# Kernel tuning notes

Hardware: AMD Instinct MI355X
Metric: run time of the kernel (lower is better)

## Reference

```python
import jax, jax.numpy as jnp
import numpy as np
import math

B, C, H, W = 16, 256, 32, 32
MPHI = 16      # GRModule projection channels
NNODE = 20     # symbol nodes
DEMB = 300     # fastText dim


def setup_inputs() -> dict:
    key = jax.random.key(0)
    ks = jax.random.split(key, 24)
    r = lambda i, shp, s=0.05: jax.random.normal(ks[i], shp, dtype=jnp.float32) * s
    return {
        'x': r(0, (B, C, H, W), 1.0),
        'emb': r(1, (NNODE, DEMB), 1.0),
        'adj': jax.random.uniform(ks[2], (NNODE, NNODE), dtype=jnp.float32),
        'wq': r(3, (DEMB, DEMB)), 'bq': r(4, (DEMB,)),
        'wk': r(5, (DEMB, DEMB)), 'bk': r(6, (DEMB,)),
        'wv': r(7, (DEMB, DEMB)), 'bv': r(8, (DEMB,)),
        'wo': r(9, (DEMB, DEMB)), 'bo': r(10, (DEMB,)),
        'phi_w': r(11, (MPHI, C)), 'phi_b': r(12, (MPHI,)),
        'glob_w': r(13, (MPHI, C)),
        'gc1_w': r(14, (DEMB, C)),
        'gc2_w': r(15, (C, C)),
        'gw_w': r(16, (C, C)),
        's2l_w': r(17, (2 * C,)), 's2l_b': r(18, (1,)),
        'final_w': r(19, (C, 2 * C)),
    }


def _attention_graph(node, wq, bq, wk, bk, wv, bv, wo, bo):
    # node: [N, 300]. Single-head self-attention, mean-pooled residual (dropout=eval).
    q = node @ wq + bq
    k = node @ wk + bk
    v = node @ wv + bv
    att = jax.nn.softmax(q @ k.T / math.sqrt(DEMB), axis=-1)
    node1 = (att @ v).mean(axis=0, keepdims=True)      # [1, 300]
    node2 = node1 @ wo + bo
    return node + node2                                 # broadcast residual


def _gr_module(x, phi_w, phi_b, glob_w):
    # x: [B, C, H, W] -> [B, HW, C]
    b = x.shape[0]
    phi = jnp.einsum('oc,bchw->bohw', phi_w, x) + phi_b[None, :, None, None]  # [B,16,H,W]
    x_phi = jax.nn.relu(phi.reshape(b, -1, MPHI))       # raw reshape, as in torch .view
    x_phi_T = jax.nn.relu(phi.reshape(b, MPHI, -1))
    g = jnp.einsum('oc,bc->bo', glob_w, x.mean(axis=(2, 3)))  # [B,16]
    # sigmoid of the diag-embedded matrix: off-diagonal becomes sigmoid(0)=0.5 (faithful)
    Dg = jax.nn.sigmoid(jax.vmap(jnp.diag)(g))          # [B,16,16]
    A = jax.nn.softmax(jnp.einsum('bpm,bmn,bnq->bpq', x_phi, Dg, x_phi_T), axis=-1)
    d = 1.0 / jnp.sqrt(A.sum(axis=2))
    d = jnp.where(jnp.isfinite(d), d, 0.0)              # nan/inf -> 0
    L = jnp.eye(A.shape[1], dtype=A.dtype) - d[:, :, None] * A * d[:, None, :]
    return jnp.einsum('bpq,bqc->bpc', L, x.reshape(b, -1, x.shape[1]))


def _normalize_adjacency(adj):
    a_hat = adj + jnp.eye(adj.shape[0], dtype=adj.dtype)
    d = 1.0 / jnp.sqrt(a_hat.sum(axis=1))
    d = jnp.where(jnp.isfinite(d), d, 0.0)
    return d[:, None] * a_hat * d[None, :]


def reference(x, emb, adj, wq, bq, wk, bk, wv, bv, wo, bo,
              phi_w, phi_b, glob_w, gc1_w, gc2_w, gw_w, s2l_w, s2l_b, final_w):
    b, c, h, w = x.shape
    # --- semantic branch: attention over word graph + 2-layer GCN ---
    ev = _attention_graph(emb, wq, bq, wk, bk, wv, bv, wo, bo)  # [N,300]
    ev = jnp.broadcast_to(ev[None], (b, NNODE, DEMB))
    adj_n = _normalize_adjacency(adj)                   # [N,N]
    g1 = jax.nn.relu(jnp.einsum('pq,bqd->bpd', adj_n, ev @ gc1_w))   # [B,N,256]
    g2 = jax.nn.relu(jnp.einsum('pq,bqd->bpd', adj_n, g1 @ gc2_w))   # [B,N,256]
    # --- local branch: GRModule Laplacian smoothing + 1x1 conv ---
    spiral = _gr_module(x, phi_w, phi_b, glob_w)        # [B,HW,C]
    spiral_map = spiral.reshape(b, h, w, c).transpose(0, 3, 1, 2)    # [B,C,H,W]
    local = jnp.einsum('oc,bchw->bohw', gw_w, spiral_map)
    # --- semantic-to-local mapping (1x1 conv over concat == two dot products) ---
    inp_flat = x.transpose(0, 2, 3, 1).reshape(b, h * w, c)          # [B,HW,C]
    w_in, w_ev = s2l_w[:c], s2l_w[c:]
    logits = (inp_flat @ w_in)[:, :, None] + (g2 @ w_ev)[:, None, :] + s2l_b[0]
    mapping = jax.nn.softmax(logits, axis=1)            # softmax over pixels
    app = jax.nn.relu(jnp.einsum('bpm,bmc->bpc', mapping, g2))       # [B,HW,C]
    app = app.reshape(b, h, w, c).transpose(0, 3, 1, 2)              # [B,C,H,W]
    # --- fuse ---
    fused = jnp.concatenate([local, app], axis=1)       # [B,2C,H,W]
    out = jnp.einsum('oc,bchw->bohw', final_w, fused)
    return jax.nn.relu(out + x)
```

## Files before the change

kernel.cpp:

```cpp
#include <hip/hip_runtime.h>
#include <hip/hip_bf16.h>

typedef __bf16 bf16_t;
typedef bf16_t bf16x8 __attribute__((ext_vector_type(8)));
typedef bf16_t bf16x4 __attribute__((ext_vector_type(4)));
typedef float  f32x4  __attribute__((ext_vector_type(4)));

#define MFMA(a,b,c) __builtin_amdgcn_mfma_f32_16x16x32_bf16((a),(b),(c),0,0,0)

__global__ __launch_bounds__(256) void k_front(
    const float* final_w, const float* gw_w, const float* emb,
    const float* wq, const float* bq, const float* wk, const float* bk,
    const float* wv, const float* bvv, const float* x,
    const float* phi_w, const float* phi_b, const float* s2l_w,
    const float* gc1_w, const float* wo, const float* bo,
    bf16_t* M16, float* qkv, bf16_t* fB, bf16_t* fBT, float* s_raw,
    float* xsump, float* csum, float* fmaxp, float* cmaxp, bf16_t* xT,
    float* E1, float* WG1, float* bg1) {
  __shared__ __align__(16) char sp[27648];
  int bid = blockIdx.x, t = threadIdx.x;
  if (bid < 256) {
    float* fw = (float*)sp;
    int o = bid, c = t;
    fw[c] = final_w[o*512 + c];
    __syncthreads();
    float acc = 0.f;
    for (int k = 0; k < 256; ++k) acc += fw[k] * gw_w[k*256 + c];
    M16[o*256 + c] = (bf16_t)acc;
    return;
  }
  if (bid < 316) {
    int id = bid - 256;
    int mat = id / 20, row = id % 20;
    const float* W  = mat == 0 ? wq : (mat == 1 ? wk : wv);
    const float* Bb = mat == 0 ? bq : (mat == 1 ? bk : bvv);
    float* er = (float*)sp;
    for (int i = t; i < 300; i += 256) er[i] = emb[row*300 + i];
    __syncthreads();
    for (int o = t; o < 300; o += 256) {
      float acc = Bb[o];
      for (int d = 0; d < 300; ++d) acc += er[d] * W[d*300 + o];
      qkv[(mat*20 + row)*300 + o] = acc;
    }
    return;
  }
  if (bid < 444) {
    int id = bid - 316;
    int b = id >> 3, role = id & 7;
    const float* xb = x + b*262144;
    float* pw = (float*)sp;
    float* wi = pw + 4096;
    float* pb = wi + 256;
    float* phs = pb + 16;
    unsigned* fmu = (unsigned*)(phs + 2304);
    unsigned* cmu = fmu + 16;
    for (int i = t; i < 4096; i += 256) pw[i] = phi_w[i];
    wi[t] = s2l_w[t];
    if (t < 16) { pb[t] = phi_b[t]; fmu[t] = 0u; }
    if (t == 0) cmu[0] = 0u;
    __syncthreads();
    int hwl = t & 127, half = t >> 7;
    int hw = role*128 + hwl;
    float ph[16];
    #pragma unroll
    for (int o = 0; o < 16; ++o) ph[o] = 0.f;
    float sacc = 0.f;
    for (int ci = 0; ci < 128; ++ci) {
      int c = half*128 + ci;
      float xv = xb[c*1024 + hw];
      sacc += wi[c] * xv;
      #pragma unroll
      for (int o = 0; o < 16; ++o) ph[o] += pw[o*256 + c] * xv;
    }
    if (half == 0) {
      #pragma unroll
      for (int o = 0; o < 16; ++o) phs[hwl*18 + o] = ph[o];
      phs[hwl*18 + 16] = sacc;
    }
    __syncthreads();
    if (half == 1) {
      #pragma unroll
      for (int o = 0; o < 16; ++o) phs[hwl*18 + o] += ph[o];
      s_raw[b*1024 + hw] = phs[hwl*18 + 16] + sacc;
    }
    __syncthreads();
    float csacc = 0.f;
    #pragma unroll
    for (int i = 0; i < 8; ++i) {
      int j = i*256 + t;
      int o = j >> 7, hl = j & 127;
      float val = fmaxf(phs[hl*18 + o] + pb[o], 0.f);
      bf16_t bv16 = (bf16_t)val;
      atomicMax(&fmu[o], __float_as_uint((float)bv16));
      fB [b*16384 + o*1024 + role*128 + hl] = bv16;
      fBT[b*16384 + (role*128 + hl)*16 + o] = bv16;
      csacc += (float)bv16;
    }
    if (half == 0) phs[hwl*18 + 17] = csacc;
    __syncthreads();
    if (half == 1) {
      float cs = phs[hwl*18 + 17] + csacc;
      csum[b*1024 + hw] = cs;
      atomicMax(cmu, __float_as_uint(cs));
    }
    if (t < 16) fmaxp[b*128 + role*16 + t] = __uint_as_float(fmu[t]);
    __syncthreads();
    if (t == 0) cmaxp[b*8 + role] = __uint_as_float(cmu[0]);
    {
      const f32x4* xr = (const f32x4*)(xb + t*1024 + role*128);
      float s4 = 0.f;
      #pragma unroll
      for (int j = 0; j < 32; ++j) { f32x4 v = xr[j]; s4 += v[0] + v[1] + v[2] + v[3]; }
      xsump[(b*8 + role)*256 + t] = s4;
    }
    return;
  }
  if (bid < 464) {
    int n = bid - 444;
    float* er = (float*)sp;
    for (int i = t; i < 300; i += 256) er[i] = emb[n*300 + i];
    __syncthreads();
    float acc = 0.f;
    for (int d = 0; d < 300; ++d) acc += er[d] * gc1_w[d*256 + t];
    E1[n*256 + t] = acc;
    return;
  }
  if (bid < 765) {
    int d0 = bid - 464;
    float* er = (float*)sp;
    if (d0 < 300) { for (int i = t; i < 300; i += 256) er[i] = wo[d0*300 + i]; }
    else          { for (int i = t; i < 300; i += 256) er[i] = bo[i]; }
    __syncthreads();
    float acc = 0.f;
    for (int e = 0; e < 300; ++e) acc += er[e] * gc1_w[e*256 + t];
    if (d0 < 300) WG1[d0*256 + t] = acc; else bg1[t] = acc;
    return;
  }
  {
    int id = bid - 765;
    int bb = id >> 6, tile = id & 63;
    int q0 = (tile >> 2) * 64, c0 = (tile & 3) * 64;
    bf16_t* tl = (bf16_t*)sp;
    const float* xbb = x + bb*262144;
    #pragma unroll
    for (int k = 0; k < 16; ++k) {
      int idx = k*256 + t, qi = idx >> 6, ci = idx & 63;
      tl[ci*74 + qi] = (bf16_t)xbb[(q0 + qi)*256 + c0 + ci];
    }
    __syncthreads();
    #pragma unroll
    for (int k = 0; k < 16; ++k) {
      int idx = k*256 + t, ci = idx >> 6, qi = idx & 63;
      xT[bb*262144 + (c0 + ci)*1024 + q0 + qi] = tl[ci*74 + qi];
    }
    return;
  }
}

__global__ __launch_bounds__(512) void k_mid1(
    const float* adj, const float* qkv, const float* E1,
    const float* glob_w, const float* xsump, const float* s_raw,
    const float* fmaxp, const float* cmaxp,
    float* n1g, float* adjng, float* rsAg, float* AE1g,
    float* dgd, float* mcol, float* fmaxb, float* cmaxb) {
  __shared__ __align__(16) float sp[12480];
  int t = threadIdx.x;
  if (blockIdx.x == 0) {
    float* A  = sp;
    float* Bs = A + 6000;
    float* att  = Bs + 6000;
    float* wsum = att + 400;
    for (int i = t; i < 6000; i += 512) { A[i] = qkv[i]; Bs[i] = qkv[6000 + i]; }
    __syncthreads();
    if (t < 400) {
      int i = t / 20, j = t % 20;
      float acc = 0.f;
      for (int d = 0; d < 300; ++d) acc += A[i*300 + d] * Bs[j*300 + d];
      att[t] = acc * 0.05773502691896258f;
    }
    __syncthreads();
    if (t < 20) {
      float m = -1e30f;
      for (int j = 0; j < 20; ++j) m = fmaxf(m, att[t*20 + j]);
      float s = 0.f;
      for (int j = 0; j < 20; ++j) { float e = __expf(att[t*20 + j] - m); att[t*20 + j] = e; s += e; }
      float inv = 1.f / s;
      for (int j = 0; j < 20; ++j) att[t*20 + j] *= inv;
    }
    __syncthreads();
    if (t < 20) {
      float s = 0.f;
      for (int i = 0; i < 20; ++i) s += att[i*20 + t];
      wsum[t] = s * 0.05f;
    }
    __syncthreads();
    if (t < 300) {
      const float* v = qkv + 12000;
      float acc = 0.f;
      for (int j = 0; j < 20; ++j) acc += wsum[j] * v[j*300 + t];
      n1g[t] = acc;
    }
    return;
  }
  if (blockIdx.x == 1) {
    float* drt = sp;
    float* an  = sp + 32;
    if (t < 20) {
      float s = 1.f;
      for (int j = 0; j < 20; ++j) s += adj[t*20 + j];
      drt[t] = rsqrtf(s);
    }
    __syncthreads();
    if (t < 400) {
      int i = t / 20, j = t % 20;
      float a = adj[t] + (i == j ? 1.f : 0.f);
      float v = drt[i] * a * drt[j];
      an[t] = v;
      adjng[t] = v;
    }
    __syncthreads();
    if (t < 20) {
      float s = 0.f;
      for (int m = 0; m < 20; ++m) s += an[t*20 + m];
      rsAg[t] = s;
    }
    if (t < 256) {
      float e[20];
      #pragma unroll
      for (int m = 0; m < 20; ++m) e[m] = E1[m*256 + t];
      for (int n = 0; n < 20; ++n) {
        float acc = 0.f;
        #pragma unroll
        for (int m = 0; m < 20; ++m) acc += an[n*20 + m] * e[m];
        AE1g[n*256 + t] = acc;
      }
    }
    return;
  }
  int b = blockIdx.x - 2;
  float* xm = sp;
  float* redm = xm + 256;
  float* reds = redm + 8;
  if (t < 256) {
    float s = 0.f;
    #pragma unroll
    for (int r = 0; r < 8; ++r) s += xsump[(b*8 + r)*256 + t];
    xm[t] = s * (1.f / 1024.f);
  }
  if (t >= 256 && t < 272) {
    int m = t - 256; float fm = 0.f;
    for (int r = 0; r < 8; ++r) fm = fmaxf(fm, fmaxp[b*128 + r*16 + m]);
    fmaxb[b*16 + m] = fm;
  }
  if (t == 272) {
    float cm = 0.f;
    for (int r = 0; r < 8; ++r) cm = fmaxf(cm, cmaxp[b*8 + r]);
    cmaxb[b] = cm;
  }
  __syncthreads();
  if (t < 16) {
    float g = 0.f;
    for (int c = 0; c < 256; ++c) g += glob_w[t*256 + c] * xm[c];
    dgd[b*16 + t] = 0.5f * tanhf(0.5f * g);
  }
  float v0 = s_raw[b*1024 + t], v1 = s_raw[b*1024 + 512 + t];
  float m = fmaxf(v0, v1);
  #pragma unroll
  for (int off = 32; off; off >>= 1) m = fmaxf(m, __shfl_xor(m, off, 64));
  int wv = t >> 6, ll = t & 63;
  if (ll == 0) redm[wv] = m;
  __syncthreads();
  float bm = redm[0];
  #pragma unroll
  for (int i = 1; i < 8; ++i) bm = fmaxf(bm, redm[i]);
  float e0 = __expf(v0 - bm), e1 = __expf(v1 - bm);
  float s2 = e0 + e1;
  #pragma unroll
  for (int off = 32; off; off >>= 1) s2 += __shfl_xor(s2, off, 64);
  if (ll == 0) reds[wv] = s2;
  __syncthreads();
  float tot = 0.f;
  #pragma unroll
  for (int i = 0; i < 8; ++i) tot += reds[i];
  float inv = 1.f / tot;
  mcol[b*1024 + t]       = e0 * inv;
  mcol[b*1024 + 512 + t] = e1 * inv;
}

__global__ __launch_bounds__(256) void k_w1(const float* n1g, const float* WG1,
                                            float* w1part) {
  int t = threadIdx.x, i = blockIdx.x, d0 = i*8;
  float acc = 0.f;
  #pragma unroll
  for (int k = 0; k < 8; ++k) {
    int d = d0 + k;
    if (d < 300) acc += n1g[d] * WG1[d*256 + t];
  }
  w1part[i*256 + t] = acc;
}

__global__ __launch_bounds__(256) void k_gu(const float* w1part,
    const float* bg1, const float* AE1g, const float* rsAg, const float* adjng,
    const float* gc2_w, const float* final_w, float* upart) {
  __shared__ float adjns[400], rsAs[32], w1s[256], h2s[640], rgs[32];
  __shared__ float g1s[5120];
  int t = threadIdx.x, c0 = blockIdx.x * 32;
  for (int i = t; i < 400; i += 256) adjns[i] = adjng[i];
  if (t < 20) rsAs[t] = rsAg[t];
  {
    float acc = bg1[t];
    #pragma unroll
    for (int i = 0; i < 38; ++i) acc += w1part[i*256 + t];
    w1s[t] = acc;
  }
  __syncthreads();
  for (int i = t; i < 5120; i += 256) {
    int n = i >> 8;
    g1s[i] = fmaxf(AE1g[i] + rsAs[n] * w1s[i & 255], 0.f);
  }
  __syncthreads();
  int cl = t & 31, ng = t >> 5;
  float a0 = 0.f, a1 = 0.f, a2 = 0.f;
  for (int d = 0; d < 256; ++d) {
    float wv = gc2_w[d*256 + c0 + cl];
    a0 += g1s[ng*256 + d] * wv;
    a1 += g1s[(ng + 8)*256 + d] * wv;
    if (ng < 4) a2 += g1s[(ng + 16)*256 + d] * wv;
  }
  h2s[ng*32 + cl] = a0;
  h2s[(ng + 8)*32 + cl] = a1;
  if (ng < 4) h2s[(ng + 16)*32 + cl] = a2;
  __syncthreads();
  if (t < 32) {
    float rga = 0.f;
    for (int n = 0; n < 20; ++n) {
      float acc = 0.f;
      #pragma unroll
      for (int m = 0; m < 20; ++m) acc += adjns[n*20 + m] * h2s[m*32 + t];
      rga += fmaxf(acc, 0.f);
    }
    rgs[t] = rga;
  }
  __syncthreads();
  {
    float acc = 0.f;
    const float* fw = final_w + t*512 + 256 + c0;
    #pragma unroll
    for (int kk = 0; kk < 32; ++kk) acc += fw[kk] * rgs[kk];
    upart[blockIdx.x*256 + t] = acc;
  }
}

__global__ __launch_bounds__(256) void k_main(const float* x, const bf16_t* fB,
    const bf16_t* fBT, const bf16_t* xT, const bf16_t* M16, const float* fmaxb,
    const float* mcol, const float* upart, const float* dgd, const float* csum,
    const float* cmaxb, float* out) {
  int flat = blockIdx.y * 32 + blockIdx.x;
  int b  = (flat & 7) * 2 + ((flat >> 3) >> 5);
  int p0 = ((flat >> 3) & 31) * 32;
  int t = threadIdx.x, w = t >> 6, l = t & 63, lr = l & 15, quad = l >> 4;
  int qh = w >> 1, ph = w & 1;
  __shared__ __align__(16) char smem[16896];
  bf16_t* PT0  = (bf16_t*)smem;
  bf16_t* e_s  = (bf16_t*)(smem + 10240);
  bf16_t* T_ls = (bf16_t*)smem;
  __shared__ float Mb_s[32], fmax_s[16], u_s[256], rsinv_s[32], dgd_s[16];
  __shared__ float c_s[1024], ha_s[32], rs_s[2][32];
  const float*  xb   = x   + b*262144;
  const bf16_t* fBb  = fB  + b*16384;
  const bf16_t* fBTb = fBT + b*16384;
  const bf16_t* xTb  = xT  + b*262144;
  for (int i = t; i < 1280; i += 256) e_s[i] = (bf16_t)0.f;
  {
    float us = 0.f;
    #pragma unroll
    for (int j = 0; j < 8; ++j) us += upart[j*256 + t];
    u_s[t] = us;
  }
  for (int i = t; i < 1024; i += 256) c_s[i] = csum[b*1024 + i];
  if (t < 16) { fmax_s[t] = fmaxb[b*16 + t]; dgd_s[t] = dgd[b*16 + t]; }
  __syncthreads();
  for (int i = t; i < 512; i += 256) {
    int p = i >> 4, m = i & 15;
    e_s[p*40 + m] = (bf16_t)((float)fBb[p0*16 + i] * dgd_s[m]);
  }
  __syncthreads();
  if (t < 32) {
    float a = 0.f;
    #pragma unroll
    for (int m = 0; m < 16; ++m) a += (float)fBb[(p0 + t)*16 + m];
    float ha = 0.5f * a;
    ha_s[t] = ha;
    float mb = ha * cmaxb[b];
    #pragma unroll
    for (int m = 0; m < 16; ++m) mb += fmaxf((float)e_s[t*40 + m], 0.f) * fmax_s[m];
    Mb_s[t] = mb;
  }
  __syncthreads();
  bf16x8 be = *(const bf16x8*)(e_s + (ph*16 + lr)*40 + quad*8);
  float mb_lane = Mb_s[ph*16 + lr];
  float ha_lane = ha_s[ph*16 + lr];
  float rs = 0.f;
  f32x4 acc[2][4];
  #pragma unroll
  for (int i = 0; i < 2; ++i)
    #pragma unroll
    for (int j = 0; j < 4; ++j) acc[i][j] = (f32x4){0.f, 0.f, 0.f, 0.f};
  bf16x8 zer;
  #pragma unroll
  for (int j = 0; j < 8; ++j) zer[j] = (bf16_t)0.f;
  bf16x8 a0[2], a0n[2];
  a0[0] = a0[1] = a0n[0] = a0n[1] = zer;
  if (quad < 2) {
    a0[0] = *(const bf16x8*)(fBTb + (qh*16 + lr)*16 + quad*8);
    a0[1] = *(const bf16x8*)(fBTb + (32 + qh*16 + lr)*16 + quad*8);
  }
  const bf16_t* xrow = xTb + (w*64 + lr)*1024 + quad*8;
  bf16x8 bv[2][4], bvn[2][4];
  #pragma unroll
  for (int k = 0; k < 2; ++k)
    #pragma unroll
    for (int cf = 0; cf < 4; ++cf)
      bv[k][cf] = *(const bf16x8*)(xrow + cf*16384 + k*32);
  int cur = 0;
  for (int u2 = 0; u2 < 16; ++u2) {
    f32x4 z = {0.f, 0.f, 0.f, 0.f};
    f32x4 s0 = MFMA(a0[0], be, z);
    f32x4 s1 = MFMA(a0[1], be, z);
    if (u2 < 15) {
      if (quad < 2) {
        a0n[0] = *(const bf16x8*)(fBTb + ((u2*2 + 2)*32 + qh*16 + lr)*16 + quad*8);
        a0n[1] = *(const bf16x8*)(fBTb + ((u2*2 + 3)*32 + qh*16 + lr)*16 + quad*8);
      }
      #pragma unroll
      for (int k = 0; k < 2; ++k)
        #pragma unroll
        for (int cf = 0; cf < 4; ++cf)
          bvn[k][cf] = *(const bf16x8*)(xrow + cf*16384 + (u2*2 + 2 + k)*32);
    }
    bf16_t* PTc = PT0 + cur*2560;
    bf16x4 pv0, pv1;
    #pragma unroll
    for (int r = 0; r < 4; ++r) {
      float S0 = s0[r] + ha_lane * c_s[(u2*2)*32 + qh*16 + quad*4 + r];
      float E0 = __expf(S0 - mb_lane);
      rs += E0; pv0[r] = (bf16_t)E0;
      float S1 = s1[r] + ha_lane * c_s[(u2*2 + 1)*32 + qh*16 + quad*4 + r];
      float E1v = __expf(S1 - mb_lane);
      rs += E1v; pv1[r] = (bf16_t)E1v;
    }
    *(bf16x4*)(PTc + (ph*16 + lr)*40 + qh*16 + quad*4)        = pv0;
    *(bf16x4*)(PTc + 1280 + (ph*16 + lr)*40 + qh*16 + quad*4) = pv1;
    __syncthreads();
    #pragma unroll
    for (int k = 0; k < 2; ++k) {
      bf16x8 ap0 = *(const bf16x8*)(PTc + k*1280 + lr*40 + quad*8);
      bf16x8 ap1 = *(const bf16x8*)(PTc + k*1280 + (16 + lr)*40 + quad*8);
      #pragma unroll
      for (int cf = 0; cf < 4; ++cf) {
        acc[0][cf] = MFMA(ap0, bv[k][cf], acc[0][cf]);
        acc[1][cf] = MFMA(ap1, bv[k][cf], acc[1][cf]);
      }
    }
    if (u2 < 15) {
      #pragma unroll
      for (int k = 0; k < 2; ++k) {
        a0[k] = a0n[k];
        #pragma unroll
        for (int cf = 0; cf < 4; ++cf) bv[k][cf] = bvn[k][cf];
      }
    }
    cur ^= 1;
  }
  rs += __shfl_xor(rs, 16, 64);
  rs += __shfl_xor(rs, 32, 64);
  if (l < 16) rs_s[qh][ph*16 + lr] = rs;
  __syncthreads();
  if (t < 32) rsinv_s[t] = 1.f / fmaxf(rs_s[0][t] + rs_s[1][t], 1e-30f);
  __syncthreads();
  #pragma unroll
  for (int pf = 0; pf < 2; ++pf)
    #pragma unroll
    for (int cf = 0; cf < 4; ++cf)
      #pragma unroll
      for (int r = 0; r < 4; ++r) {
        int p = pf*16 + quad*4 + r;
        int c = w*64 + cf*16 + lr;
        float tv = xb[(p0 + p)*256 + c] - acc[pf][cf][r] * rsinv_s[p];
        T_ls[p*264 + c] = (bf16_t)tv;
      }
  __syncthreads();
  f32x4 acc2[4][2];
  #pragma unroll
  for (int i = 0; i < 4; ++i)
    #pragma unroll
    for (int j = 0; j < 2; ++j) acc2[i][j] = (f32x4){0.f, 0.f, 0.f, 0.f};
  for (int c0 = 0; c0 < 256; c0 += 32) {
    bf16x8 am[4], bt[2];
    #pragma unroll
    for (int of = 0; of < 4; ++of)
      am[of] = *(const bf16x8*)(M16 + (w*64 + of*16 + lr)*256 + c0 + quad*8);
    #pragma unroll
    for (int pf = 0; pf < 2; ++pf)
      bt[pf] = *(const bf16x8*)(T_ls + (pf*16 + lr)*264 + c0 + quad*8);
    #pragma unroll
    for (int of = 0; of < 4; ++of)
      #pragma unroll
      for (int pf = 0; pf < 2; ++pf) acc2[of][pf] = MFMA(am[of], bt[pf], acc2[of][pf]);
  }
  float* outb = out + b*262144;
  #pragma unroll
  for (int of = 0; of < 4; ++of)
    #pragma unroll
    for (int pf = 0; pf < 2; ++pf)
      #pragma unroll
      for (int r = 0; r < 4; ++r) {
        int o = w*64 + of*16 + quad*4 + r;
        int pg = p0 + pf*16 + lr;
        float v = acc2[of][pf][r] + mcol[b*1024 + pg] * u_s[o] + xb[o*1024 + pg];
        outb[o*1024 + pg] = fmaxf(v, 0.f);
      }
}


extern "C" void kernel_launch(void* const* d_in, const int* in_sizes, int n_in,
                              void* d_out, int out_size, void* d_ws, size_t ws_size,
                              hipStream_t stream) {
  (void)in_sizes; (void)n_in; (void)out_size; (void)ws_size;
  const float* x       = (const float*)d_in[0];
  const float* emb     = (const float*)d_in[1];
  const float* adj     = (const float*)d_in[2];
  const float* wq      = (const float*)d_in[3];
  const float* bq      = (const float*)d_in[4];
  const float* wk      = (const float*)d_in[5];
  const float* bk      = (const float*)d_in[6];
  const float* wv      = (const float*)d_in[7];
  const float* bv      = (const float*)d_in[8];
  const float* wo      = (const float*)d_in[9];
  const float* bo      = (const float*)d_in[10];
  const float* phi_w   = (const float*)d_in[11];
  const float* phi_b   = (const float*)d_in[12];
  const float* glob_w  = (const float*)d_in[13];
  const float* gc1_w   = (const float*)d_in[14];
  const float* gc2_w   = (const float*)d_in[15];
  const float* gw_w    = (const float*)d_in[16];
  const float* s2l_w   = (const float*)d_in[17];
  const float* final_w = (const float*)d_in[19];
  float* out = (float*)d_out;

  float* W = (float*)d_ws;
  float* qkv    = W + 0;
  float* xsump  = W + 18048;
  float* s_raw  = W + 50816;
  float* mcol   = W + 67200;
  float* fmaxb  = W + 83584;
  float* dgd    = W + 83840;
  float* csum   = W + 84096;
  float* cmaxb  = W + 100480;
  float* fmaxp  = W + 100544;
  float* cmaxp  = W + 102592;
  float* E1     = W + 102720;
  float* WG1    = W + 107840;
  float* bg1    = W + 184640;
  float* n1     = W + 184896;
  float* adjn   = W + 185216;
  float* rsA    = W + 185664;
  float* AE1    = W + 185728;
  float* upart  = W + 190848;
  float* w1part = W + 192896;
  bf16_t* M16 = (bf16_t*)((char*)d_ws + 851968);
  bf16_t* fB  = (bf16_t*)((char*)d_ws + 983040);
  bf16_t* fBT = (bf16_t*)((char*)d_ws + 1507328);
  bf16_t* xT  = (bf16_t*)((char*)d_ws + 2031616);

  k_front<<<1789, 256, 0, stream>>>(final_w, gw_w, emb, wq, bq, wk, bk, wv, bv, x,
                                    phi_w, phi_b, s2l_w, gc1_w, wo, bo,
                                    M16, qkv, fB, fBT, s_raw, xsump, csum,
                                    fmaxp, cmaxp, xT, E1, WG1, bg1);
  k_mid1<<<18, 512, 0, stream>>>(adj, qkv, E1, glob_w, xsump, s_raw,
                                 fmaxp, cmaxp,
                                 n1, adjn, rsA, AE1, dgd, mcol, fmaxb, cmaxb);
  k_w1<<<38, 256, 0, stream>>>(n1, WG1, w1part);
  k_gu<<<8, 256, 0, stream>>>(w1part, bg1, AE1, rsA, adjn, gc2_w, final_w, upart);
  k_main<<<dim3(32, 16), 256, 0, stream>>>(x, fB, fBT, xT, M16, fmaxb, mcol, upart,
                                           dgd, csum, cmaxb, out);
}
```

Measured before the change: 232.4 us.

## Split k_gu over more blocks; restructure k_main softmax-attention to per-wave register shuffles

k_gu now runs 32 blocks of 8 output columns each instead of 8 blocks of 32. It stages the gc2_w slice in shared memory and uses a padded g1 layout. k_main is reorganized so each wave owns a 16-pixel by 128-channel tile and computes all query steps itself. The exp'd attention probabilities are passed into the A operand through cross-lane shuffles instead of a shared-memory transpose with a block barrier each step, and row sums are reduced within the wave. In exchange it drops the software prefetch of the next step's operands and duplicates the score MFMA and exp work across the two channel-half waves.

```diff
diff --git a/kernel.cpp b/kernel.cpp
--- a/kernel.cpp
+++ b/kernel.cpp
@@ -302,42 +302,45 @@
 __global__ __launch_bounds__(256) void k_gu(const float* w1part,
     const float* bg1, const float* AE1g, const float* rsAg, const float* adjng,
     const float* gc2_w, const float* final_w, float* upart) {
-  __shared__ float adjns[400], rsAs[32], w1s[256], h2s[640], rgs[32];
-  __shared__ float g1s[5120];
-  int t = threadIdx.x, c0 = blockIdx.x * 32;
+  __shared__ float adjns[400], rsAs[32], w1s[256], h2s[176], rgs[8];
+  __shared__ float g1s[20*260];
+  __shared__ float gs2[2048];
+  int t = threadIdx.x, c0 = blockIdx.x * 8;
   for (int i = t; i < 400; i += 256) adjns[i] = adjng[i];
   if (t < 20) rsAs[t] = rsAg[t];
+  #pragma unroll
+  for (int k2 = 0; k2 < 8; ++k2) {
+    int idx = k2*256 + t, d = idx >> 3, cl = idx & 7;
+    gs2[idx] = gc2_w[d*256 + c0 + cl];
+  }
   {
     float acc = bg1[t];
     #pragma unroll
     for (int i = 0; i < 38; ++i) acc += w1part[i*256 + t];
     w1s[t] = acc;
   }
-  __syncthreads();
-  for (int i = t; i < 5120; i += 256) {
-    int n = i >> 8;
-    g1s[i] = fmaxf(AE1g[i] + rsAs[n] * w1s[i & 255], 0.f);
-  }
-  __syncthreads();
-  int cl = t & 31, ng = t >> 5;
-  float a0 = 0.f, a1 = 0.f, a2 = 0.f;
-  for (int d = 0; d < 256; ++d) {
-    float wv = gc2_w[d*256 + c0 + cl];
-    a0 += g1s[ng*256 + d] * wv;
-    a1 += g1s[(ng + 8)*256 + d] * wv;
-    if (ng < 4) a2 += g1s[(ng + 16)*256 + d] * wv;
-  }
-  h2s[ng*32 + cl] = a0;
-  h2s[(ng + 8)*32 + cl] = a1;
-  if (ng < 4) h2s[(ng + 16)*32 + cl] = a2;
-  __syncthreads();
-  if (t < 32) {
+  float ae[20];
+  #pragma unroll
+  for (int k2 = 0; k2 < 20; ++k2) ae[k2] = AE1g[k2*256 + t];
+  __syncthreads();
+  #pragma unroll
+  for (int k2 = 0; k2 < 20; ++k2)
+    g1s[k2*260 + t] = fmaxf(ae[k2] + rsAs[k2] * w1s[t], 0.f);
+  __syncthreads();
+  int cl = t & 7, n = t >> 3;
+  if (n < 20) {
+    float acc = 0.f;
+    for (int d = 0; d < 256; ++d) acc += g1s[n*260 + d] * gs2[d*8 + cl];
+    h2s[n*8 + cl] = acc;
+  }
+  __syncthreads();
+  if (t < 8) {
     float rga = 0.f;
-    for (int n = 0; n < 20; ++n) {
-      float acc = 0.f;
-      #pragma unroll
-      for (int m = 0; m < 20; ++m) acc += adjns[n*20 + m] * h2s[m*32 + t];
-      rga += fmaxf(acc, 0.f);
+    for (int nn = 0; nn < 20; ++nn) {
+      float a2 = 0.f;
+      #pragma unroll
+      for (int m = 0; m < 20; ++m) a2 += adjns[nn*20 + m] * h2s[m*8 + t];
+      rga += fmaxf(a2, 0.f);
     }
     rgs[t] = rga;
   }
@@ -346,7 +349,7 @@
     float acc = 0.f;
     const float* fw = final_w + t*512 + 256 + c0;
     #pragma unroll
-    for (int kk = 0; kk < 32; ++kk) acc += fw[kk] * rgs[kk];
+    for (int kk = 0; kk < 8; ++kk) acc += fw[kk] * rgs[kk];
     upart[blockIdx.x*256 + t] = acc;
   }
 }
@@ -359,13 +362,12 @@
   int b  = (flat & 7) * 2 + ((flat >> 3) >> 5);
   int p0 = ((flat >> 3) & 31) * 32;
   int t = threadIdx.x, w = t >> 6, l = t & 63, lr = l & 15, quad = l >> 4;
-  int qh = w >> 1, ph = w & 1;
+  int ph = w & 1, ch = w >> 1;
   __shared__ __align__(16) char smem[16896];
-  bf16_t* PT0  = (bf16_t*)smem;
-  bf16_t* e_s  = (bf16_t*)(smem + 10240);
+  bf16_t* e_s  = (bf16_t*)smem;
   bf16_t* T_ls = (bf16_t*)smem;
-  __shared__ float Mb_s[32], fmax_s[16], u_s[256], rsinv_s[32], dgd_s[16];
-  __shared__ float c_s[1024], ha_s[32], rs_s[2][32];
+  __shared__ float Mb_s[32], fmax_s[16], u_s[256], dgd_s[16];
+  __shared__ float c_s[1024], ha_s[32];
   const float*  xb   = x   + b*262144;
   const bf16_t* fBb  = fB  + b*16384;
   const bf16_t* fBTb = fBT + b*16384;
@@ -374,7 +376,7 @@
   {
     float us = 0.f;
     #pragma unroll
-    for (int j = 0; j < 8; ++j) us += upart[j*256 + t];
+    for (int j = 0; j < 32; ++j) us += upart[j*256 + t];
     u_s[t] = us;
   }
   for (int i = t; i < 1024; i += 256) c_s[i] = csum[b*1024 + i];
@@ -401,94 +403,79 @@
   float mb_lane = Mb_s[ph*16 + lr];
   float ha_lane = ha_s[ph*16 + lr];
   float rs = 0.f;
-  f32x4 acc[2][4];
-  #pragma unroll
-  for (int i = 0; i < 2; ++i)
-    #pragma unroll
-    for (int j = 0; j < 4; ++j) acc[i][j] = (f32x4){0.f, 0.f, 0.f, 0.f};
+  f32x4 acc[8];
+  #pragma unroll
+  for (int j = 0; j < 8; ++j) acc[j] = (f32x4){0.f, 0.f, 0.f, 0.f};
   bf16x8 zer;
   #pragma unroll
   for (int j = 0; j < 8; ++j) zer[j] = (bf16_t)0.f;
-  bf16x8 a0[2], a0n[2];
-  a0[0] = a0[1] = a0n[0] = a0n[1] = zer;
-  if (quad < 2) {
-    a0[0] = *(const bf16x8*)(fBTb + (qh*16 + lr)*16 + quad*8);
-    a0[1] = *(const bf16x8*)(fBTb + (32 + qh*16 + lr)*16 + quad*8);
-  }
-  const bf16_t* xrow = xTb + (w*64 + lr)*1024 + quad*8;
-  bf16x8 bv[2][4], bvn[2][4];
-  #pragma unroll
-  for (int k = 0; k < 2; ++k)
-    #pragma unroll
-    for (int cf = 0; cf < 4; ++cf)
-      bv[k][cf] = *(const bf16x8*)(xrow + cf*16384 + k*32);
-  int cur = 0;
-  for (int u2 = 0; u2 < 16; ++u2) {
+  const bf16_t* xrow = xTb + (ch*128 + lr)*1024 + quad*8;
+  int srcLo = ((quad & 1) << 5) + lr;
+  int srcHi = srcLo + 16;
+  bool hi = quad >= 2;
+  for (int st = 0; st < 32; ++st) {
+    bf16x8 a0 = zer, a1 = zer;
+    if (quad < 2) {
+      a0 = *(const bf16x8*)(fBTb + (st*32 + lr)*16 + quad*8);
+      a1 = *(const bf16x8*)(fBTb + (st*32 + 16 + lr)*16 + quad*8);
+    }
+    bf16x8 bv[8];
+    #pragma unroll
+    for (int cf = 0; cf < 8; ++cf)
+      bv[cf] = *(const bf16x8*)(xrow + cf*16384 + st*32);
     f32x4 z = {0.f, 0.f, 0.f, 0.f};
-    f32x4 s0 = MFMA(a0[0], be, z);
-    f32x4 s1 = MFMA(a0[1], be, z);
-    if (u2 < 15) {
-      if (quad < 2) {
-        a0n[0] = *(const bf16x8*)(fBTb + ((u2*2 + 2)*32 + qh*16 + lr)*16 + quad*8);
-        a0n[1] = *(const bf16x8*)(fBTb + ((u2*2 + 3)*32 + qh*16 + lr)*16 + quad*8);
-      }
-      #pragma unroll
-      for (int k = 0; k < 2; ++k)
-        #pragma unroll
-        for (int cf = 0; cf < 4; ++cf)
-          bvn[k][cf] = *(const bf16x8*)(xrow + cf*16384 + (u2*2 + 2 + k)*32);
-    }
-    bf16_t* PTc = PT0 + cur*2560;
-    bf16x4 pv0, pv1;
+    f32x4 s0 = MFMA(a0, be, z);
+    f32x4 s1 = MFMA(a1, be, z);
+    float E0[4], E1v[4];
     #pragma unroll
     for (int r = 0; r < 4; ++r) {
-      float S0 = s0[r] + ha_lane * c_s[(u2*2)*32 + qh*16 + quad*4 + r];
-      float E0 = __expf(S0 - mb_lane);
-      rs += E0; pv0[r] = (bf16_t)E0;
-      float S1 = s1[r] + ha_lane * c_s[(u2*2 + 1)*32 + qh*16 + quad*4 + r];
-      float E1v = __expf(S1 - mb_lane);
-      rs += E1v; pv1[r] = (bf16_t)E1v;
-    }
-    *(bf16x4*)(PTc + (ph*16 + lr)*40 + qh*16 + quad*4)        = pv0;
-    *(bf16x4*)(PTc + 1280 + (ph*16 + lr)*40 + qh*16 + quad*4) = pv1;
-    __syncthreads();
-    #pragma unroll
-    for (int k = 0; k < 2; ++k) {
-      bf16x8 ap0 = *(const bf16x8*)(PTc + k*1280 + lr*40 + quad*8);
-      bf16x8 ap1 = *(const bf16x8*)(PTc + k*1280 + (16 + lr)*40 + quad*8);
-      #pragma unroll
-      for (int cf = 0; cf < 4; ++cf) {
-        acc[0][cf] = MFMA(ap0, bv[k][cf], acc[0][cf]);
-        acc[1][cf] = MFMA(ap1, bv[k][cf], acc[1][cf]);
-      }
-    }
-    if (u2 < 15) {
-      #pragma unroll
-      for (int k = 0; k < 2; ++k) {
-        a0[k] = a0n[k];
-        #pragma unroll
-        for (int cf = 0; cf < 4; ++cf) bv[k][cf] = bvn[k][cf];
-      }
-    }
-    cur ^= 1;
+      float S0 = s0[r] + ha_lane * c_s[st*32 + quad*4 + r];
+      float S1 = s1[r] + ha_lane * c_s[st*32 + 16 + quad*4 + r];
+      E0[r] = __expf(S0 - mb_lane);
+      E1v[r] = __expf(S1 - mb_lane);
+      rs += E0[r] + E1v[r];
+    }
+    unsigned P0, P1, P2, P3;
+    {
+      union { bf16_t h[2]; unsigned u; } pk;
+      pk.h[0] = (bf16_t)E0[0];  pk.h[1] = (bf16_t)E0[1];  P0 = pk.u;
+      pk.h[0] = (bf16_t)E0[2];  pk.h[1] = (bf16_t)E0[3];  P1 = pk.u;
+      pk.h[0] = (bf16_t)E1v[0]; pk.h[1] = (bf16_t)E1v[1]; P2 = pk.u;
+      pk.h[0] = (bf16_t)E1v[2]; pk.h[1] = (bf16_t)E1v[3]; P3 = pk.u;
+    }
+    unsigned xA = (unsigned)__shfl((int)P0, srcLo, 64);
+    unsigned xB = (unsigned)__shfl((int)P2, srcLo, 64);
+    unsigned yA = (unsigned)__shfl((int)P1, srcLo, 64);
+    unsigned yB = (unsigned)__shfl((int)P3, srcLo, 64);
+    unsigned zA = (unsigned)__shfl((int)P0, srcHi, 64);
+    unsigned zB = (unsigned)__shfl((int)P2, srcHi, 64);
+    unsigned wA = (unsigned)__shfl((int)P1, srcHi, 64);
+    unsigned wB = (unsigned)__shfl((int)P3, srcHi, 64);
+    union { unsigned u[4]; bf16x8 v; } af;
+    af.u[0] = hi ? xB : xA;
+    af.u[1] = hi ? yB : yA;
+    af.u[2] = hi ? zB : zA;
+    af.u[3] = hi ? wB : wA;
+    bf16x8 ap = af.v;
+    #pragma unroll
+    for (int cf = 0; cf < 8; ++cf) acc[cf] = MFMA(ap, bv[cf], acc[cf]);
   }
   rs += __shfl_xor(rs, 16, 64);
   rs += __shfl_xor(rs, 32, 64);
-  if (l < 16) rs_s[qh][ph*16 + lr] = rs;
-  __syncthreads();
-  if (t < 32) rsinv_s[t] = 1.f / fmaxf(rs_s[0][t] + rs_s[1][t], 1e-30f);
-  __syncthreads();
-  #pragma unroll
-  for (int pf = 0; pf < 2; ++pf)
-    #pragma unroll
-    for (int cf = 0; cf < 4; ++cf)
-      #pragma unroll
-      for (int r = 0; r < 4; ++r) {
-        int p = pf*16 + quad*4 + r;
-        int c = w*64 + cf*16 + lr;
-        float tv = xb[(p0 + p)*256 + c] - acc[pf][cf][r] * rsinv_s[p];
-        T_ls[p*264 + c] = (bf16_t)tv;
-      }
+  float rsinv = 1.f / fmaxf(rs, 1e-30f);
+  float rsv[4];
+  #pragma unroll
+  for (int r = 0; r < 4; ++r) rsv[r] = __shfl(rsinv, quad*4 + r, 64);
+  __syncthreads();
+  #pragma unroll
+  for (int cf = 0; cf < 8; ++cf)
+    #pragma unroll
+    for (int r = 0; r < 4; ++r) {
+      int p = ph*16 + quad*4 + r;
+      int c = ch*128 + cf*16 + lr;
+      float tv = xb[(p0 + p)*256 + c] - acc[cf][r] * rsv[r];
+      T_ls[p*264 + c] = (bf16_t)tv;
+    }
   __syncthreads();
   f32x4 acc2[4][2];
   #pragma unroll
@@ -567,7 +554,7 @@
   float* rsA    = W + 185664;
   float* AE1    = W + 185728;
   float* upart  = W + 190848;
-  float* w1part = W + 192896;
+  float* w1part = W + 199040;
   bf16_t* M16 = (bf16_t*)((char*)d_ws + 851968);
   bf16_t* fB  = (bf16_t*)((char*)d_ws + 983040);
   bf16_t* fBT = (bf16_t*)((char*)d_ws + 1507328);
@@ -581,7 +568,7 @@
                                  fmaxp, cmaxp,
                                  n1, adjn, rsA, AE1, dgd, mcol, fmaxb, cmaxb);
   k_w1<<<38, 256, 0, stream>>>(n1, WG1, w1part);
-  k_gu<<<8, 256, 0, stream>>>(w1part, bg1, AE1, rsA, adjn, gc2_w, final_w, upart);
+  k_gu<<<32, 256, 0, stream>>>(w1part, bg1, AE1, rsA, adjn, gc2_w, final_w, upart);
   k_main<<<dim3(32, 16), 256, 0, stream>>>(x, fB, fBT, xT, M16, fmaxb, mcol, upart,
                                            dgd, csum, cmaxb, out);
 }
```

Result: no change. 228.9 us (-1.5%).
